# Performance work log

Measured on AMD Instinct MI355X. Metric: run time of the kernel, lower is better.

## Reference

```python
import jax, jax.numpy as jnp
import numpy as np

B, T, D_IN, H = 32, 1024, 512, 768
FORGET_BIAS = 1.0  # TF LSTMCell default


def lstm_scan(x_tbd, W, b, peep):
    """Run a peephole LSTM over x_tbd [T, B, D]; returns hidden states [T, B, H].

    Matches tf LSTMCell(use_peepholes=True): gate packing (i, j, f, o),
    peepholes on i/f from c_prev and on o from new c, forget_bias added to f.
    """
    h_units = b.shape[0] // 4
    w_i, w_f, w_o = peep[0], peep[1], peep[2]

    def step(carry, xt):
        c, h = carry
        z = jnp.concatenate([xt, h], axis=-1) @ W + b  # [B, 4H]
        i, j, f, o = jnp.split(z, 4, axis=-1)
        i = jax.nn.sigmoid(i + w_i * c)
        f = jax.nn.sigmoid(f + FORGET_BIAS + w_f * c)
        c_new = f * c + i * jnp.tanh(j)
        o = jax.nn.sigmoid(o + w_o * c_new)
        h_new = o * jnp.tanh(c_new)
        return (c_new, h_new), h_new

    bsz = x_tbd.shape[1]
    init = (jnp.zeros((bsz, h_units), x_tbd.dtype),
            jnp.zeros((bsz, h_units), x_tbd.dtype))
    _, hs = jax.lax.scan(step, init, x_tbd)
    return hs


def setup_inputs() -> dict:
    key = jax.random.key(0)
    ks = jax.random.split(key, 6)
    scale = 0.1  # ~ tf.random_uniform_initializer(-0.1, 0.1)
    x = jax.random.normal(ks[0], (B, T, D_IN), dtype=jnp.float32)
    W_fw = jax.random.uniform(ks[1], (D_IN + H, 4 * H), jnp.float32, -scale, scale)
    W_bw = jax.random.uniform(ks[2], (D_IN + H, 4 * H), jnp.float32, -scale, scale)
    b_fw = jnp.zeros((4 * H,), jnp.float32)
    b_bw = jnp.zeros((4 * H,), jnp.float32)
    peep_fw = jax.random.uniform(ks[3], (3, H), jnp.float32, -scale, scale)
    peep_bw = jax.random.uniform(ks[4], (3, H), jnp.float32, -scale, scale)
    return {"x": x, "W_fw": W_fw, "b_fw": b_fw, "peep_fw": peep_fw,
            "W_bw": W_bw, "b_bw": b_bw, "peep_bw": peep_bw}


def reference(x, W_fw, b_fw, peep_fw, W_bw, b_bw, peep_bw):
    x_tbd = jnp.transpose(x, (1, 0, 2))  # [T, B, D]
    hs_fw = lstm_scan(x_tbd, W_fw, b_fw, peep_fw)            # [T, B, H]
    hs_bw = lstm_scan(x_tbd[::-1], W_bw, b_bw, peep_bw)[::-1]  # [T, B, H]
    out = jnp.concatenate([hs_fw, hs_bw], axis=-1)           # [T, B, 2H]
    # static_bidirectional_rnn + reshape -> [B, n_steps, 2*n_hidden]
    return jnp.transpose(out, (1, 0, 2))
```

## Files before the change

### kernel.cpp

```cpp
#include <hip/hip_runtime.h>
#include <stdint.h>

#define TS   1024
#define NB   32
#define DIN  512
#define HU   768
#define NWG  32
#define UPW  24
#define XPAD 520
#define HPAD 772
#define SPIN_MAX 16384

typedef _Float16 f16x8 __attribute__((ext_vector_type(8)));
typedef float f32x16 __attribute__((ext_vector_type(16)));
typedef unsigned int u32;
typedef unsigned long long u64;
typedef u32 u32x4 __attribute__((ext_vector_type(4)));

__device__ __forceinline__ u32 f2h_bits(float f) {
  _Float16 h = (_Float16)f;
  return (u32)__builtin_bit_cast(unsigned short, h);
}

__global__ void lstm_init_k(u64* hb) {
  hb[blockIdx.x * 256 + threadIdx.x] = 0ull;
}

__global__ void lstm_xpose_k(const float* __restrict__ x, unsigned short* __restrict__ xh) {
  int idx = blockIdx.x * 256 + threadIdx.x;
  int d4 = idx & 127;
  int t  = (idx >> 7) & 1023;
  int b  = idx >> 17;
  float4 v = *(const float4*)(x + ((size_t)(b * TS + t) * DIN + d4 * 4));
  ushort4 o;
  o.x = (unsigned short)f2h_bits(v.x); o.y = (unsigned short)f2h_bits(v.y);
  o.z = (unsigned short)f2h_bits(v.z); o.w = (unsigned short)f2h_bits(v.w);
  *(ushort4*)(xh + ((size_t)(t * NB + b) * DIN + d4 * 4)) = o;
}

#define BAR_LGKM() do { asm volatile("s_waitcnt lgkmcnt(0)" ::: "memory"); \
  __builtin_amdgcn_sched_barrier(0); __builtin_amdgcn_s_barrier(); \
  __builtin_amdgcn_sched_barrier(0); } while (0)

__global__ __launch_bounds__(256, 1) void lstm_persist_k(
    const float* __restrict__ Wfw, const float* __restrict__ bfw, const float* __restrict__ pfw,
    const float* __restrict__ Wbw, const float* __restrict__ bbw, const float* __restrict__ pbw,
    const unsigned short* __restrict__ xh,
    u64* hb, float* __restrict__ out)
{
  __shared__ __align__(16) unsigned short As[NB * XPAD];
  __shared__ __align__(16) unsigned short Hs[NB * HPAD];
  __shared__ __align__(16) float Zs[4][NB][100];

  const int tid = threadIdx.x;
  const int dir = (blockIdx.x >= NWG) ? 1 : 0;
  const int gg  = blockIdx.x & (NWG - 1);

  const float* W    = dir ? Wbw : Wfw;
  const float* bias = dir ? bbw : bfw;
  const float* peep = dir ? pbw : pfw;
  u64* hslot = hb + (size_t)dir * 2 * 8192;
  const int u0 = gg * UPW;

  const int lane  = tid & 63;
  const int wq    = tid >> 6;
  const int colc  = lane & 31;
  const int khalf = lane >> 5;
  const int arow  = colc;
  const int eb    = tid >> 3;
  const int ep    = tid & 7;

  f16x8 wfr[3][20];
#pragma unroll
  for (int ct = 0; ct < 3; ++ct) {
    const int gcol = (colc & 3) * HU + u0 + 8 * ct + (colc >> 2);
#pragma unroll
    for (int m = 0; m < 20; ++m) {
      const int k0 = (8 * m + 4 * khalf + wq) * 8;
#pragma unroll
      for (int j = 0; j < 8; ++j)
        wfr[ct][m][j] = (_Float16)W[(size_t)(k0 + j) * 3072 + gcol];
    }
  }

  float bi[3], bj[3], bfc[3], bo[3], pi[3], pfc[3], po[3], cst[3];
#pragma unroll
  for (int q = 0; q < 3; ++q) {
    const int U = u0 + 3 * ep + q;
    bi[q] = bias[U]; bj[q] = bias[HU + U]; bfc[q] = bias[2 * HU + U]; bo[q] = bias[3 * HU + U];
    pi[q] = peep[U]; pfc[q] = peep[HU + U]; po[q] = peep[2 * HU + U];
    cst[q] = 0.0f;
  }

  {
    const unsigned short* x0 = xh + (size_t)(dir ? (TS - 1) : 0) * (NB * DIN);
    u32x4 t[8];
#pragma unroll
    for (int k = 0; k < 8; ++k) t[k] = *(const u32x4*)(x0 + (tid + 256 * k) * 8);
#pragma unroll
    for (int k = 0; k < 8; ++k) {
      const int idx = tid + 256 * k;
      *(u32x4*)(&As[(idx >> 6) * XPAD + (idx & 63) * 8]) = t[k];
    }
  }
  BAR_LGKM();

  const int hsBase0 = 1544 * ((tid >> 2) & 31) + 48 * (tid >> 7) + 6 * ((2 * tid) & 7);

  u32x4 xr[8];

  for (int s = 0; s < TS; ++s) {
    const int t_in = dir ? (TS - 1 - s) : s;
    const u32 tag = (u32)s;
    const char* hp = (const char*)(hslot + (size_t)(s & 1) * 8192) + 16 * tid;
    u64* hdst = hslot + (size_t)((s + 1) & 1) * 8192;

    u32x4 hw[16];
#pragma unroll
    for (int k = 0; k < 16; ++k)
      asm volatile("global_load_dwordx4 %0, %1, off sc0 sc1"
                   : "=v"(hw[k]) : "v"(hp + 4096 * k) : "memory");

    if (s + 1 < TS) {
      const unsigned short* xnb = xh + (size_t)(dir ? (TS - 2 - s) : (s + 1)) * (NB * DIN);
#pragma unroll
      for (int k = 0; k < 8; ++k) xr[k] = *(const u32x4*)(xnb + (tid + 256 * k) * 8);
    }

    f32x16 a0, a1, a2;
#pragma unroll
    for (int r = 0; r < 16; ++r) { a0[r] = 0.f; a1[r] = 0.f; a2[r] = 0.f; }
#pragma unroll
    for (int m = 0; m < 8; ++m) {
      const int c = 8 * m + 4 * khalf + wq;
      const f16x8 av = *(const f16x8*)(&As[arow * XPAD + c * 8]);
      a0 = __builtin_amdgcn_mfma_f32_32x32x16_f16(av, wfr[0][m], a0, 0, 0, 0);
      a1 = __builtin_amdgcn_mfma_f32_32x32x16_f16(av, wfr[1][m], a1, 0, 0, 0);
      a2 = __builtin_amdgcn_mfma_f32_32x32x16_f16(av, wfr[2][m], a2, 0, 0, 0);
    }

    {
      u32 freshmask = 0;
      int it = 0;
      while (true) {
        if (it == 0) asm volatile("s_waitcnt vmcnt(8)" ::: "memory");
        else         asm volatile("s_waitcnt vmcnt(0)" ::: "memory");
        __builtin_amdgcn_sched_barrier(0);
        u32 stale = 0;
#pragma unroll
        for (int k = 0; k < 16; ++k) {
          if (!(freshmask & (1u << k))) {
            const u32 badk = ((hw[k][1] >> 16) ^ tag) | ((hw[k][3] >> 16) ^ tag);
            if (__all((int)(badk == 0))) freshmask |= 1u << k;
            else stale |= 1u << k;
          }
        }
        if (stale == 0 || ++it >= SPIN_MAX) break;
        if (it > 2) __builtin_amdgcn_s_sleep(1);
#pragma unroll
        for (int k = 0; k < 16; ++k)
          if (stale & (1u << k))
            asm volatile("global_load_dwordx4 %0, %1, off sc0 sc1"
                         : "=v"(hw[k]) : "v"(hp + 4096 * k) : "memory");
      }
    }

    {
      char* dp0 = (char*)Hs + hsBase0;
#pragma unroll
      for (int k = 0; k < 16; ++k) {
        const u32 xw = hw[k][0], yw = hw[k][1], zw = hw[k][2], ww = hw[k][3];
        char* dp = dp0 + 96 * k;
        *(u32*)(dp)     = xw;
        *(u32*)(dp + 4) = (yw & 0xFFFFu) | (zw << 16);
        *(u32*)(dp + 8) = (zw >> 16) | (ww << 16);
      }
    }
    BAR_LGKM();

#pragma unroll
    for (int m = 8; m < 20; ++m) {
      const int c = 8 * m + 4 * khalf + wq;
      const f16x8 av = *(const f16x8*)((char*)Hs + arow * (2 * HPAD) + (c - 64) * 16);
      a0 = __builtin_amdgcn_mfma_f32_32x32x16_f16(av, wfr[0][m], a0, 0, 0, 0);
      a1 = __builtin_amdgcn_mfma_f32_32x32x16_f16(av, wfr[1][m], a1, 0, 0, 0);
      a2 = __builtin_amdgcn_mfma_f32_32x32x16_f16(av, wfr[2][m], a2, 0, 0, 0);
    }

#pragma unroll
    for (int r = 0; r < 16; ++r) {
      const int prow = (r & 3) + 8 * (r >> 2) + 4 * khalf;
      Zs[wq][prow][colc]      = a0[r];
      Zs[wq][prow][32 + colc] = a1[r];
      Zs[wq][prow][64 + colc] = a2[r];
    }
    if (s + 1 < TS) {
#pragma unroll
      for (int k = 0; k < 8; ++k) {
        const int idx = tid + 256 * k;
        *(u32x4*)(&As[(idx >> 6) * XPAD + (idx & 63) * 8]) = xr[k];
      }
    }
    BAR_LGKM();

    float hn[3];
#pragma unroll
    for (int q = 0; q < 3; ++q) {
      const int uu = 3 * ep + q;
      float zi = 0.f, zj = 0.f, zf = 0.f, zo = 0.f;
#pragma unroll
      for (int qq = 0; qq < 4; ++qq) {
        const float4 zp = *(const float4*)(&Zs[qq][eb][uu * 4]);
        zi += zp.x; zj += zp.y; zf += zp.z; zo += zp.w;
      }
      const float ig = 1.f / (1.f + __expf(-(zi + bi[q] + pi[q] * cst[q])));
      const float fg = 1.f / (1.f + __expf(-(zf + bfc[q] + 1.f + pfc[q] * cst[q])));
      const float jt = 1.f - 2.f / (__expf(2.f * (zj + bj[q])) + 1.f);
      const float cn = fg * cst[q] + ig * jt;
      const float og = 1.f / (1.f + __expf(-(zo + bo[q] + po[q] * cn)));
      hn[q] = og * (1.f - 2.f / (__expf(2.f * cn) + 1.f));
      cst[q] = cn;
    }

    if (s < TS - 1) {
      const u64 pk = (u64)f2h_bits(hn[0])
                   | ((u64)f2h_bits(hn[1]) << 16)
                   | ((u64)f2h_bits(hn[2]) << 32)
                   | ((u64)(u32)(s + 1) << 48);
      __hip_atomic_store(hdst + gg * 256 + tid, pk,
                         __ATOMIC_RELAXED, __HIP_MEMORY_SCOPE_AGENT);
    }
    {
      float* op = out + ((size_t)eb * TS + t_in) * 1536 + dir * HU + u0 + 3 * ep;
      op[0] = hn[0]; op[1] = hn[1]; op[2] = hn[2];
    }
  }
}

extern "C" void kernel_launch(void* const* d_in, const int* in_sizes, int n_in,
                              void* d_out, int out_size, void* d_ws, size_t ws_size,
                              hipStream_t stream) {
  const float* x   = (const float*)d_in[0];
  const float* Wfw = (const float*)d_in[1];
  const float* bfw = (const float*)d_in[2];
  const float* pfw = (const float*)d_in[3];
  const float* Wbw = (const float*)d_in[4];
  const float* bbw = (const float*)d_in[5];
  const float* pbw = (const float*)d_in[6];
  float* out = (float*)d_out;

  char* ws = (char*)d_ws;
  unsigned short* xh = (unsigned short*)ws;
  u64* hb            = (u64*)(ws + 33554432);

  lstm_init_k<<<128, 256, 0, stream>>>(hb);
  lstm_xpose_k<<<16384, 256, 0, stream>>>(x, xh);
  lstm_persist_k<<<dim3(2 * NWG), dim3(256), 0, stream>>>(Wfw, bfw, pfw, Wbw, bbw, pbw,
                                                          xh, hb, out);
}
```

Measured before the change: 5.471 ms.

## Interleave forward and backward directions in each workgroup with 16x16 MFMA tiles

Each of the 64 workgroups now handles 12 hidden units for both directions instead of 24 units for one direction. The forward and backward steps are interleaved so that one direction's hidden-state polling and exchange overlaps the other direction's compute. The change also switches to 16x16x32 MFMA tiles and streams x directly into LDS with global_load_lds. The intent is to hide inter-workgroup synchronisation latency on the serial recurrence. In exchange, each workgroup runs two serial phases per step, and half the threads sit idle during the gate computation.

```diff
diff --git a/kernel.cpp b/kernel.cpp
--- a/kernel.cpp
+++ b/kernel.cpp
@@ -5,17 +5,19 @@
 #define NB   32
 #define DIN  512
 #define HU   768
-#define NWG  32
-#define UPW  24
-#define XPAD 520
-#define HPAD 772
+#define UPW  12
+#define XROWB 1048
+#define HROWB 1560
 #define SPIN_MAX 16384
 
 typedef _Float16 f16x8 __attribute__((ext_vector_type(8)));
-typedef float f32x16 __attribute__((ext_vector_type(16)));
+typedef float f32x4 __attribute__((ext_vector_type(4)));
 typedef unsigned int u32;
 typedef unsigned long long u64;
+typedef u32 u32x2 __attribute__((ext_vector_type(2)));
 typedef u32 u32x4 __attribute__((ext_vector_type(4)));
+using gas_u32 = u32 __attribute__((address_space(1)));
+using las_u32 = u32 __attribute__((address_space(3)));
 
 __device__ __forceinline__ u32 f2h_bits(float f) {
   _Float16 h = (_Float16)f;
@@ -38,7 +40,7 @@
   *(ushort4*)(xh + ((size_t)(t * NB + b) * DIN + d4 * 4)) = o;
 }
 
-#define BAR_LGKM() do { asm volatile("s_waitcnt lgkmcnt(0)" ::: "memory"); \
+#define BARRIER() do { asm volatile("s_waitcnt lgkmcnt(0)" ::: "memory"); \
   __builtin_amdgcn_sched_barrier(0); __builtin_amdgcn_s_barrier(); \
   __builtin_amdgcn_sched_barrier(0); } while (0)
 
@@ -48,192 +50,329 @@
     const unsigned short* __restrict__ xh,
     u64* hb, float* __restrict__ out)
 {
-  __shared__ __align__(16) unsigned short As[NB * XPAD];
-  __shared__ __align__(16) unsigned short Hs[NB * HPAD];
-  __shared__ __align__(16) float Zs[4][NB][100];
-
-  const int tid = threadIdx.x;
-  const int dir = (blockIdx.x >= NWG) ? 1 : 0;
-  const int gg  = blockIdx.x & (NWG - 1);
-
-  const float* W    = dir ? Wbw : Wfw;
-  const float* bias = dir ? bbw : bfw;
-  const float* peep = dir ? pbw : pfw;
-  u64* hslot = hb + (size_t)dir * 2 * 8192;
-  const int u0 = gg * UPW;
-
-  const int lane  = tid & 63;
-  const int wq    = tid >> 6;
-  const int colc  = lane & 31;
-  const int khalf = lane >> 5;
-  const int arow  = colc;
-  const int eb    = tid >> 3;
-  const int ep    = tid & 7;
-
-  f16x8 wfr[3][20];
-#pragma unroll
-  for (int ct = 0; ct < 3; ++ct) {
-    const int gcol = (colc & 3) * HU + u0 + 8 * ct + (colc >> 2);
-#pragma unroll
-    for (int m = 0; m < 20; ++m) {
-      const int k0 = (8 * m + 4 * khalf + wq) * 8;
-#pragma unroll
-      for (int j = 0; j < 8; ++j)
-        wfr[ct][m][j] = (_Float16)W[(size_t)(k0 + j) * 3072 + gcol];
-    }
-  }
-
-  float bi[3], bj[3], bfc[3], bo[3], pi[3], pfc[3], po[3], cst[3];
+  __shared__ __align__(16) char AsF[NB * XROWB];
+  __shared__ __align__(16) char AsB[NB * XROWB];
+  __shared__ __align__(16) char Hst[NB * HROWB];
+  __shared__ __align__(16) float Zs[4][NB][52];
+
+  const int tid  = threadIdx.x;
+  const int gg   = blockIdx.x;
+  const int lane = tid & 63;
+  const int wq   = tid >> 6;
+  const int l15  = lane & 15;
+  const int l4   = lane >> 4;
+  const int ep   = tid & 7;
+  const int eb   = tid >> 3;
+  const int u0   = gg * UPW;
+
+  u64* hbF = hb;
+  u64* hbB = hb + 16384;
+
+  f16x8 wfr[2][3][10];
+#pragma unroll
+  for (int d = 0; d < 2; ++d) {
+    const float* W = d ? Wbw : Wfw;
+#pragma unroll
+    for (int ct = 0; ct < 3; ++ct) {
+      const int gcol = (l15 & 3) * HU + u0 + 4 * ct + (l15 >> 2);
+#pragma unroll
+      for (int i = 0; i < 10; ++i) {
+        const int k0 = (4 * i + wq) * 32 + l4 * 8;
+#pragma unroll
+        for (int j = 0; j < 8; ++j)
+          wfr[d][ct][i][j] = (_Float16)W[(size_t)(k0 + j) * 3072 + gcol];
+      }
+    }
+  }
+
+  float biF[3], bjF[3], bfF[3], boF[3], piF[3], pfF[3], poF[3], cstF[3];
+  float biB[3], bjB[3], bfB[3], boB[3], piB[3], pfB[3], poB[3], cstB[3];
 #pragma unroll
   for (int q = 0; q < 3; ++q) {
-    const int U = u0 + 3 * ep + q;
-    bi[q] = bias[U]; bj[q] = bias[HU + U]; bfc[q] = bias[2 * HU + U]; bo[q] = bias[3 * HU + U];
-    pi[q] = peep[U]; pfc[q] = peep[HU + U]; po[q] = peep[2 * HU + U];
-    cst[q] = 0.0f;
-  }
+    int uu = 3 * ep + q; if (uu > 11) uu = 11;
+    const int U = u0 + uu;
+    biF[q] = bfw[U]; bjF[q] = bfw[HU + U]; bfF[q] = bfw[2 * HU + U]; boF[q] = bfw[3 * HU + U];
+    piF[q] = pfw[U]; pfF[q] = pfw[HU + U]; poF[q] = pfw[2 * HU + U]; cstF[q] = 0.f;
+    biB[q] = bbw[U]; bjB[q] = bbw[HU + U]; bfB[q] = bbw[2 * HU + U]; boB[q] = bbw[3 * HU + U];
+    piB[q] = pbw[U]; pfB[q] = pbw[HU + U]; poB[q] = pbw[2 * HU + U]; cstB[q] = 0.f;
+  }
+
+  const int hsBase0 = HROWB * ((tid & 63) >> 1) + 24 * (tid >> 6) + 12 * (tid & 1);
 
   {
-    const unsigned short* x0 = xh + (size_t)(dir ? (TS - 1) : 0) * (NB * DIN);
-    u32x4 t[8];
-#pragma unroll
-    for (int k = 0; k < 8; ++k) t[k] = *(const u32x4*)(x0 + (tid + 256 * k) * 8);
-#pragma unroll
-    for (int k = 0; k < 8; ++k) {
-      const int idx = tid + 256 * k;
-      *(u32x4*)(&As[(idx >> 6) * XPAD + (idx & 63) * 8]) = t[k];
-    }
-  }
-  BAR_LGKM();
-
-  const int hsBase0 = 1544 * ((tid >> 2) & 31) + 48 * (tid >> 7) + 6 * ((2 * tid) & 7);
-
-  u32x4 xr[8];
-
-  for (int s = 0; s < TS; ++s) {
-    const int t_in = dir ? (TS - 1 - s) : s;
-    const u32 tag = (u32)s;
-    const char* hp = (const char*)(hslot + (size_t)(s & 1) * 8192) + 16 * tid;
-    u64* hdst = hslot + (size_t)((s + 1) & 1) * 8192;
-
-    u32x4 hw[16];
+    const unsigned short* xF = xh;
+    const unsigned short* xB = xh + (size_t)(TS - 1) * (NB * DIN);
+#pragma unroll
+    for (int cc = 0; cc < 8; ++cc) {
+      const int row = wq * 8 + cc;
+      __builtin_amdgcn_global_load_lds((const gas_u32*)(xF + row * DIN + lane * 8),
+                                       (las_u32*)(AsF + row * XROWB), 16, 0, 0);
+      __builtin_amdgcn_global_load_lds((const gas_u32*)(xB + row * DIN + lane * 8),
+                                       (las_u32*)(AsB + row * XROWB), 16, 0, 0);
+    }
+  }
+  __builtin_amdgcn_sched_barrier(0);
+
+  u32x4 hw[16];
+  {
+    const char* hp = (const char*)hbF + 16 * tid;
 #pragma unroll
     for (int k = 0; k < 16; ++k)
       asm volatile("global_load_dwordx4 %0, %1, off sc0 sc1"
                    : "=v"(hw[k]) : "v"(hp + 4096 * k) : "memory");
-
-    if (s + 1 < TS) {
-      const unsigned short* xnb = xh + (size_t)(dir ? (TS - 2 - s) : (s + 1)) * (NB * DIN);
-#pragma unroll
-      for (int k = 0; k < 8; ++k) xr[k] = *(const u32x4*)(xnb + (tid + 256 * k) * 8);
-    }
-
-    f32x16 a0, a1, a2;
-#pragma unroll
-    for (int r = 0; r < 16; ++r) { a0[r] = 0.f; a1[r] = 0.f; a2[r] = 0.f; }
-#pragma unroll
-    for (int m = 0; m < 8; ++m) {
-      const int c = 8 * m + 4 * khalf + wq;
-      const f16x8 av = *(const f16x8*)(&As[arow * XPAD + c * 8]);
-      a0 = __builtin_amdgcn_mfma_f32_32x32x16_f16(av, wfr[0][m], a0, 0, 0, 0);
-      a1 = __builtin_amdgcn_mfma_f32_32x32x16_f16(av, wfr[1][m], a1, 0, 0, 0);
-      a2 = __builtin_amdgcn_mfma_f32_32x32x16_f16(av, wfr[2][m], a2, 0, 0, 0);
-    }
-
-    {
-      u32 freshmask = 0;
-      int it = 0;
+  }
+  __builtin_amdgcn_sched_barrier(0);
+
+  for (int s = 0; s < TS; ++s) {
+    const u32 tag  = (u32)s;
+    const u32 ntag = (u32)(s + 1);
+    const char* hpF = (const char*)(hbF + (size_t)(s & 1) * 8192) + 16 * tid;
+    const char* hpB = (const char*)(hbB + (size_t)(s & 1) * 8192) + 16 * tid;
+    u64* wdF = hbF + (size_t)((s + 1) & 1) * 8192;
+    u64* wdB = hbB + (size_t)((s + 1) & 1) * 8192;
+
+    if (s == 0) asm volatile("s_waitcnt vmcnt(0)" ::: "memory");
+    else        asm volatile("s_waitcnt vmcnt(12)" ::: "memory");
+    __builtin_amdgcn_sched_barrier(0);
+    {
+      u32 fresh = 0; int it = 0;
       while (true) {
-        if (it == 0) asm volatile("s_waitcnt vmcnt(8)" ::: "memory");
-        else         asm volatile("s_waitcnt vmcnt(0)" ::: "memory");
-        __builtin_amdgcn_sched_barrier(0);
         u32 stale = 0;
 #pragma unroll
         for (int k = 0; k < 16; ++k) {
-          if (!(freshmask & (1u << k))) {
+          if (!((fresh >> k) & 1)) {
             const u32 badk = ((hw[k][1] >> 16) ^ tag) | ((hw[k][3] >> 16) ^ tag);
-            if (__all((int)(badk == 0))) freshmask |= 1u << k;
-            else stale |= 1u << k;
+            if (__all((int)(badk == 0))) fresh |= 1u << k; else stale |= 1u << k;
           }
         }
         if (stale == 0 || ++it >= SPIN_MAX) break;
         if (it > 2) __builtin_amdgcn_s_sleep(1);
 #pragma unroll
         for (int k = 0; k < 16; ++k)
-          if (stale & (1u << k))
+          if ((stale >> k) & 1)
             asm volatile("global_load_dwordx4 %0, %1, off sc0 sc1"
-                         : "=v"(hw[k]) : "v"(hp + 4096 * k) : "memory");
-      }
-    }
-
-    {
-      char* dp0 = (char*)Hs + hsBase0;
-#pragma unroll
-      for (int k = 0; k < 16; ++k) {
-        const u32 xw = hw[k][0], yw = hw[k][1], zw = hw[k][2], ww = hw[k][3];
-        char* dp = dp0 + 96 * k;
-        *(u32*)(dp)     = xw;
-        *(u32*)(dp + 4) = (yw & 0xFFFFu) | (zw << 16);
-        *(u32*)(dp + 8) = (zw >> 16) | (ww << 16);
-      }
-    }
-    BAR_LGKM();
-
-#pragma unroll
-    for (int m = 8; m < 20; ++m) {
-      const int c = 8 * m + 4 * khalf + wq;
-      const f16x8 av = *(const f16x8*)((char*)Hs + arow * (2 * HPAD) + (c - 64) * 16);
-      a0 = __builtin_amdgcn_mfma_f32_32x32x16_f16(av, wfr[0][m], a0, 0, 0, 0);
-      a1 = __builtin_amdgcn_mfma_f32_32x32x16_f16(av, wfr[1][m], a1, 0, 0, 0);
-      a2 = __builtin_amdgcn_mfma_f32_32x32x16_f16(av, wfr[2][m], a2, 0, 0, 0);
-    }
-
-#pragma unroll
-    for (int r = 0; r < 16; ++r) {
-      const int prow = (r & 3) + 8 * (r >> 2) + 4 * khalf;
-      Zs[wq][prow][colc]      = a0[r];
-      Zs[wq][prow][32 + colc] = a1[r];
-      Zs[wq][prow][64 + colc] = a2[r];
-    }
-    if (s + 1 < TS) {
-#pragma unroll
-      for (int k = 0; k < 8; ++k) {
-        const int idx = tid + 256 * k;
-        *(u32x4*)(&As[(idx >> 6) * XPAD + (idx & 63) * 8]) = xr[k];
-      }
-    }
-    BAR_LGKM();
-
-    float hn[3];
-#pragma unroll
-    for (int q = 0; q < 3; ++q) {
-      const int uu = 3 * ep + q;
-      float zi = 0.f, zj = 0.f, zf = 0.f, zo = 0.f;
-#pragma unroll
-      for (int qq = 0; qq < 4; ++qq) {
-        const float4 zp = *(const float4*)(&Zs[qq][eb][uu * 4]);
-        zi += zp.x; zj += zp.y; zf += zp.z; zo += zp.w;
-      }
-      const float ig = 1.f / (1.f + __expf(-(zi + bi[q] + pi[q] * cst[q])));
-      const float fg = 1.f / (1.f + __expf(-(zf + bfc[q] + 1.f + pfc[q] * cst[q])));
-      const float jt = 1.f - 2.f / (__expf(2.f * (zj + bj[q])) + 1.f);
-      const float cn = fg * cst[q] + ig * jt;
-      const float og = 1.f / (1.f + __expf(-(zo + bo[q] + po[q] * cn)));
-      hn[q] = og * (1.f - 2.f / (__expf(2.f * cn) + 1.f));
-      cst[q] = cn;
-    }
-
-    if (s < TS - 1) {
-      const u64 pk = (u64)f2h_bits(hn[0])
-                   | ((u64)f2h_bits(hn[1]) << 16)
-                   | ((u64)f2h_bits(hn[2]) << 32)
-                   | ((u64)(u32)(s + 1) << 48);
-      __hip_atomic_store(hdst + gg * 256 + tid, pk,
-                         __ATOMIC_RELAXED, __HIP_MEMORY_SCOPE_AGENT);
-    }
-    {
-      float* op = out + ((size_t)eb * TS + t_in) * 1536 + dir * HU + u0 + 3 * ep;
-      op[0] = hn[0]; op[1] = hn[1]; op[2] = hn[2];
-    }
+                         : "=v"(hw[k]) : "v"(hpF + 4096 * k) : "memory");
+        asm volatile("s_waitcnt vmcnt(0)" ::: "memory");
+        __builtin_amdgcn_sched_barrier(0);
+      }
+    }
+
+#pragma unroll
+    for (int k = 0; k < 16; ++k) {
+      char* dp = Hst + hsBase0 + 96 * k;
+      *(u32*)(dp)     = hw[k][0];
+      *(u32*)(dp + 4) = (hw[k][1] & 0xFFFFu) | (hw[k][2] << 16);
+      *(u32*)(dp + 8) = (hw[k][2] >> 16) | (hw[k][3] << 16);
+    }
+    __builtin_amdgcn_sched_barrier(0);
+
+#pragma unroll
+    for (int k = 0; k < 16; ++k)
+      asm volatile("global_load_dwordx4 %0, %1, off sc0 sc1"
+                   : "=v"(hw[k]) : "v"(hpB + 4096 * k) : "memory");
+    __builtin_amdgcn_sched_barrier(0);
+
+    BARRIER();
+
+    {
+      f32x4 acc[2][3];
+#pragma unroll
+      for (int rb = 0; rb < 2; ++rb)
+#pragma unroll
+        for (int ct = 0; ct < 3; ++ct)
+#pragma unroll
+          for (int r = 0; r < 4; ++r) acc[rb][ct][r] = 0.f;
+#pragma unroll
+      for (int i = 0; i < 10; ++i) {
+        const int c = 4 * i + wq;
+#pragma unroll
+        for (int rb = 0; rb < 2; ++rb) {
+          const int row = rb * 16 + l15;
+          const char* src = (c < 16) ? (AsF + row * XROWB + c * 64 + l4 * 16)
+                                     : (Hst + row * HROWB + (c - 16) * 64 + l4 * 16);
+          const f16x8 af = *(const f16x8*)src;
+          acc[rb][0] = __builtin_amdgcn_mfma_f32_16x16x32_f16(af, wfr[0][0][i], acc[rb][0], 0, 0, 0);
+          acc[rb][1] = __builtin_amdgcn_mfma_f32_16x16x32_f16(af, wfr[0][1][i], acc[rb][1], 0, 0, 0);
+          acc[rb][2] = __builtin_amdgcn_mfma_f32_16x16x32_f16(af, wfr[0][2][i], acc[rb][2], 0, 0, 0);
+        }
+      }
+#pragma unroll
+      for (int rb = 0; rb < 2; ++rb)
+#pragma unroll
+        for (int ct = 0; ct < 3; ++ct)
+#pragma unroll
+          for (int r = 0; r < 4; ++r)
+            Zs[wq][rb * 16 + l4 * 4 + r][16 * ct + l15] = acc[rb][ct][r];
+    }
+    BARRIER();
+
+    float hnF[3];
+    if (ep < 4) {
+#pragma unroll
+      for (int q = 0; q < 3; ++q) {
+        const int uu = 3 * ep + q;
+        float zi = 0.f, zj = 0.f, zf = 0.f, zo = 0.f;
+#pragma unroll
+        for (int qq = 0; qq < 4; ++qq) {
+          const float4 zp = *(const float4*)(&Zs[qq][eb][4 * uu]);
+          zi += zp.x; zj += zp.y; zf += zp.z; zo += zp.w;
+        }
+        const float ig = 1.f / (1.f + __expf(-(zi + biF[q] + piF[q] * cstF[q])));
+        const float fg = 1.f / (1.f + __expf(-(zf + bfF[q] + 1.f + pfF[q] * cstF[q])));
+        const float jt = 1.f - 2.f / (__expf(2.f * (zj + bjF[q])) + 1.f);
+        const float cn = fg * cstF[q] + ig * jt;
+        const float og = 1.f / (1.f + __expf(-(zo + boF[q] + poF[q] * cn)));
+        hnF[q] = og * (1.f - 2.f / (__expf(2.f * cn) + 1.f));
+        cstF[q] = cn;
+      }
+    }
+    __builtin_amdgcn_sched_barrier(0);
+
+    {
+      const int tn = (s + 1 < TS) ? (s + 1) : (TS - 1);
+      const unsigned short* xn = xh + (size_t)tn * (NB * DIN);
+#pragma unroll
+      for (int cc = 0; cc < 8; ++cc) {
+        const int row = wq * 8 + cc;
+        __builtin_amdgcn_global_load_lds((const gas_u32*)(xn + row * DIN + lane * 8),
+                                         (las_u32*)(AsF + row * XROWB), 16, 0, 0);
+      }
+      if (ep < 4) {
+        u32x2 pk;
+        pk[0] = f2h_bits(hnF[0]) | (f2h_bits(hnF[1]) << 16);
+        pk[1] = f2h_bits(hnF[2]) | (ntag << 16);
+        const u64* wp = wdF + gg * 128 + eb * 4 + ep;
+        asm volatile("global_store_dwordx2 %0, %1, off sc0 sc1" :: "v"(wp), "v"(pk) : "memory");
+        float* op = out + ((size_t)eb * TS + s) * 1536 + u0 + 3 * ep;
+        asm volatile("global_store_dword %0, %1, off" :: "v"(op), "v"(hnF[0]) : "memory");
+        asm volatile("global_store_dword %0, %1, off" :: "v"(op + 1), "v"(hnF[1]) : "memory");
+        asm volatile("global_store_dword %0, %1, off" :: "v"(op + 2), "v"(hnF[2]) : "memory");
+      } else {
+      }
+    }
+    __builtin_amdgcn_sched_barrier(0);
+
+    asm volatile("s_waitcnt vmcnt(12)" ::: "memory");
+    __builtin_amdgcn_sched_barrier(0);
+    {
+      u32 fresh = 0; int it = 0;
+      while (true) {
+        u32 stale = 0;
+#pragma unroll
+        for (int k = 0; k < 16; ++k) {
+          if (!((fresh >> k) & 1)) {
+            const u32 badk = ((hw[k][1] >> 16) ^ tag) | ((hw[k][3] >> 16) ^ tag);
+            if (__all((int)(badk == 0))) fresh |= 1u << k; else stale |= 1u << k;
+          }
+        }
+        if (stale == 0 || ++it >= SPIN_MAX) break;
+        if (it > 2) __builtin_amdgcn_s_sleep(1);
+#pragma unroll
+        for (int k = 0; k < 16; ++k)
+          if ((stale >> k) & 1)
+            asm volatile("global_load_dwordx4 %0, %1, off sc0 sc1"
+                         : "=v"(hw[k]) : "v"(hpB + 4096 * k) : "memory");
+        asm volatile("s_waitcnt vmcnt(0)" ::: "memory");
+        __builtin_amdgcn_sched_barrier(0);
+      }
+    }
+
+#pragma unroll
+    for (int k = 0; k < 16; ++k) {
+      char* dp = Hst + hsBase0 + 96 * k;
+      *(u32*)(dp)     = hw[k][0];
+      *(u32*)(dp + 4) = (hw[k][1] & 0xFFFFu) | (hw[k][2] << 16);
+      *(u32*)(dp + 8) = (hw[k][2] >> 16) | (hw[k][3] << 16);
+    }
+    __builtin_amdgcn_sched_barrier(0);
+
+    {
+      const char* hpFn = (const char*)(hbF + (size_t)((s + 1) & 1) * 8192) + 16 * tid;
+#pragma unroll
+      for (int k = 0; k < 16; ++k)
+        asm volatile("global_load_dwordx4 %0, %1, off sc0 sc1"
+                     : "=v"(hw[k]) : "v"(hpFn + 4096 * k) : "memory");
+    }
+    __builtin_amdgcn_sched_barrier(0);
+
+    BARRIER();
+
+    {
+      f32x4 acc[2][3];
+#pragma unroll
+      for (int rb = 0; rb < 2; ++rb)
+#pragma unroll
+        for (int ct = 0; ct < 3; ++ct)
+#pragma unroll
+          for (int r = 0; r < 4; ++r) acc[rb][ct][r] = 0.f;
+#pragma unroll
+      for (int i = 0; i < 10; ++i) {
+        const int c = 4 * i + wq;
+#pragma unroll
+        for (int rb = 0; rb < 2; ++rb) {
+          const int row = rb * 16 + l15;
+          const char* src = (c < 16) ? (AsB + row * XROWB + c * 64 + l4 * 16)
+                                     : (Hst + row * HROWB + (c - 16) * 64 + l4 * 16);
+          const f16x8 af = *(const f16x8*)src;
+          acc[rb][0] = __builtin_amdgcn_mfma_f32_16x16x32_f16(af, wfr[1][0][i], acc[rb][0], 0, 0, 0);
+          acc[rb][1] = __builtin_amdgcn_mfma_f32_16x16x32_f16(af, wfr[1][1][i], acc[rb][1], 0, 0, 0);
+          acc[rb][2] = __builtin_amdgcn_mfma_f32_16x16x32_f16(af, wfr[1][2][i], acc[rb][2], 0, 0, 0);
+        }
+      }
+#pragma unroll
+      for (int rb = 0; rb < 2; ++rb)
+#pragma unroll
+        for (int ct = 0; ct < 3; ++ct)
+#pragma unroll
+          for (int r = 0; r < 4; ++r)
+            Zs[wq][rb * 16 + l4 * 4 + r][16 * ct + l15] = acc[rb][ct][r];
+    }
+    BARRIER();
+
+    {
+      const int tb = TS - 1 - s;
+      float hnB[3];
+      if (ep < 4) {
+#pragma unroll
+        for (int q = 0; q < 3; ++q) {
+          const int uu = 3 * ep + q;
+          float zi = 0.f, zj = 0.f, zf = 0.f, zo = 0.f;
+#pragma unroll
+          for (int qq = 0; qq < 4; ++qq) {
+            const float4 zp = *(const float4*)(&Zs[qq][eb][4 * uu]);
+            zi += zp.x; zj += zp.y; zf += zp.z; zo += zp.w;
+          }
+          const float ig = 1.f / (1.f + __expf(-(zi + biB[q] + piB[q] * cstB[q])));
+          const float fg = 1.f / (1.f + __expf(-(zf + bfB[q] + 1.f + pfB[q] * cstB[q])));
+          const float jt = 1.f - 2.f / (__expf(2.f * (zj + bjB[q])) + 1.f);
+          const float cn = fg * cstB[q] + ig * jt;
+          const float og = 1.f / (1.f + __expf(-(zo + boB[q] + poB[q] * cn)));
+          hnB[q] = og * (1.f - 2.f / (__expf(2.f * cn) + 1.f));
+          cstB[q] = cn;
+        }
+      }
+      __builtin_amdgcn_sched_barrier(0);
+      const int tn = (s + 1 < TS) ? (TS - 2 - s) : 0;
+      const unsigned short* xn = xh + (size_t)tn * (NB * DIN);
+#pragma unroll
+      for (int cc = 0; cc < 8; ++cc) {
+        const int row = wq * 8 + cc;
+        __builtin_amdgcn_global_load_lds((const gas_u32*)(xn + row * DIN + lane * 8),
+                                         (las_u32*)(AsB + row * XROWB), 16, 0, 0);
+      }
+      if (ep < 4) {
+        u32x2 pk;
+        pk[0] = f2h_bits(hnB[0]) | (f2h_bits(hnB[1]) << 16);
+        pk[1] = f2h_bits(hnB[2]) | (ntag << 16);
+        const u64* wp = wdB + gg * 128 + eb * 4 + ep;
+        asm volatile("global_store_dwordx2 %0, %1, off sc0 sc1" :: "v"(wp), "v"(pk) : "memory");
+        float* op = out + ((size_t)eb * TS + tb) * 1536 + HU + u0 + 3 * ep;
+        asm volatile("global_store_dword %0, %1, off" :: "v"(op), "v"(hnB[0]) : "memory");
+        asm volatile("global_store_dword %0, %1, off" :: "v"(op + 1), "v"(hnB[1]) : "memory");
+        asm volatile("global_store_dword %0, %1, off" :: "v"(op + 2), "v"(hnB[2]) : "memory");
+      }
+    }
+    __builtin_amdgcn_sched_barrier(0);
   }
 }
 
@@ -255,6 +394,6 @@
 
   lstm_init_k<<<128, 256, 0, stream>>>(hb);
   lstm_xpose_k<<<16384, 256, 0, stream>>>(x, xh);
-  lstm_persist_k<<<dim3(2 * NWG), dim3(256), 0, stream>>>(Wfw, bfw, pfw, Wbw, bbw, pbw,
-                                                          xh, hb, out);
-}
+  lstm_persist_k<<<dim3(64), dim3(256), 0, stream>>>(Wfw, bfw, pfw, Wbw, bbw, pbw,
+                                                     xh, hb, out);
+}
```

Measured after the change: 10.31 ms. 1.89x slower.
